# Kernel optimization log

Hardware: AMD Instinct MI355X
Metric: run time of the kernel (lower is better)

## Reference

```python
import jax, jax.numpy as jnp
import numpy as np

EPS = 1e-06


def setup_inputs() -> dict:
    key = jax.random.key(0)
    k1, k2, k3, k4 = jax.random.split(key, 4)
    b, n, h, w = 16, 32, 256, 256
    pd = jax.random.uniform(k1, (b, h, w), dtype=jnp.float32)
    gt = jax.random.uniform(k2, (b, h, w), dtype=jnp.float32)
    pd_mask = jax.random.randint(k3, (b, n, h, w), 0, 2, dtype=jnp.int32)
    gt_mask = jax.random.randint(k4, (b, n, h, w), 0, 2, dtype=jnp.int32)
    return {"pd": pd, "gt": gt, "pd_mask": pd_mask, "gt_mask": gt_mask}


def reference(pd, gt, pd_mask, gt_mask):
    pdm = pd_mask.astype(bool)
    gtm = gt_mask.astype(bool)
    and_m = jnp.logical_and(pdm, gtm)            # pd & gt
    xor_m = jnp.logical_and(pdm, jnp.logical_not(gtm))  # (pd|gt) ^ gt == pd & ~gt
    f = pd.dtype
    # segmented masked sums over (h,w) for every (b, n) instance, fully vectorized
    inter = jnp.einsum('bhw,bnhw->bn', pd, and_m.astype(f))
    union = (jnp.einsum('bhw,bnhw->bn', gt, gtm.astype(f))
             + jnp.einsum('bhw,bnhw->bn', pd, xor_m.astype(f)))
    loss = inter / (union + EPS)
    return 1.0 - jnp.mean(loss)
```

## Files before the change

kernel.cpp:

```cpp
#include <hip/hip_runtime.h>

#define B 16
#define N 32
#define HW 65536
#define CHUNKS 4
#define CHUNK (HW / CHUNKS)
#define PAIRS (B * N)
#define NBLK (PAIRS * CHUNKS)
#define EPS 1e-6f


__global__ __launch_bounds__(256, 4) void iou_partial_kernel(
    const float* __restrict__ pd, const float* __restrict__ gt,
    const int* __restrict__ pdm, const int* __restrict__ gtm,
    float2* __restrict__ ws)
{
    const int blk   = (blockIdx.x & 7) * (NBLK / 8) + (blockIdx.x >> 3);
    const int pair  = blk >> 2;
    const int chunk = blk & 3;
    const int b     = pair >> 5;
    const int t     = threadIdx.x;

    const int base = chunk * CHUNK;
    const float4* __restrict__ pdp = (const float4*)(pd + (size_t)b * HW + base);
    const float4* __restrict__ gtp = (const float4*)(gt + (size_t)b * HW + base);
    const int4*   __restrict__ pmp = (const int4*)(pdm + (size_t)pair * HW + base);
    const int4*   __restrict__ gmp = (const int4*)(gtm + (size_t)pair * HW + base);

    float inter = 0.0f, uni = 0.0f;

    #pragma unroll
    for (int o = 0; o < 4; ++o) {
        float4 p[4], g[4];
        int4  pm[4], gm[4];
        #pragma unroll
        for (int u = 0; u < 4; ++u) {
            const int i = (o * 4 + u) * 256 + t;
            pm[u] = pmp[i];
            gm[u] = gmp[i];
            p[u]  = pdp[i];
            g[u]  = gtp[i];
        }
        #pragma unroll
        for (int u = 0; u < 4; ++u) {
            inter += (pm[u].x & gm[u].x) ? p[u].x : 0.0f;
            inter += (pm[u].y & gm[u].y) ? p[u].y : 0.0f;
            inter += (pm[u].z & gm[u].z) ? p[u].z : 0.0f;
            inter += (pm[u].w & gm[u].w) ? p[u].w : 0.0f;

            uni += (gm[u].x ? g[u].x : 0.0f) + ((pm[u].x & ~gm[u].x) ? p[u].x : 0.0f);
            uni += (gm[u].y ? g[u].y : 0.0f) + ((pm[u].y & ~gm[u].y) ? p[u].y : 0.0f);
            uni += (gm[u].z ? g[u].z : 0.0f) + ((pm[u].z & ~gm[u].z) ? p[u].z : 0.0f);
            uni += (gm[u].w ? g[u].w : 0.0f) + ((pm[u].w & ~gm[u].w) ? p[u].w : 0.0f);
        }
    }

    #pragma unroll
    for (int o = 32; o > 0; o >>= 1) {
        inter += __shfl_down(inter, o, 64);
        uni   += __shfl_down(uni, o, 64);
    }

    __shared__ float s_i[4], s_u[4];
    const int wave = t >> 6, lane = t & 63;
    if (lane == 0) { s_i[wave] = inter; s_u[wave] = uni; }
    __syncthreads();
    if (t == 0) {
        ws[blk] = make_float2(s_i[0] + s_i[1] + s_i[2] + s_i[3],
                              s_u[0] + s_u[1] + s_u[2] + s_u[3]);
    }
}

__global__ __launch_bounds__(512) void iou_final_kernel(
    const float2* __restrict__ ws, float* __restrict__ out)
{
    const int t = threadIdx.x;
    float I = 0.0f, U = 0.0f;
    #pragma unroll
    for (int c = 0; c < CHUNKS; ++c) {
        float2 v = ws[t * CHUNKS + c];
        I += v.x; U += v.y;
    }
    float loss = I / (U + EPS);

    #pragma unroll
    for (int o = 32; o > 0; o >>= 1)
        loss += __shfl_down(loss, o, 64);

    __shared__ float s[8];
    const int wave = t >> 6, lane = t & 63;
    if (lane == 0) s[wave] = loss;
    __syncthreads();
    if (t == 0) {
        float sum = 0.0f;
        #pragma unroll
        for (int w = 0; w < 8; ++w) sum += s[w];
        out[0] = 1.0f - sum / (float)PAIRS;
    }
}

extern "C" void kernel_launch(void* const* d_in, const int* in_sizes, int n_in,
                              void* d_out, int out_size, void* d_ws, size_t ws_size,
                              hipStream_t stream) {
    const float* pd  = (const float*)d_in[0];
    const float* gt  = (const float*)d_in[1];
    const int*   pdm = (const int*)d_in[2];
    const int*   gtm = (const int*)d_in[3];
    float* out = (float*)d_out;
    float2* ws = (float2*)d_ws;

    iou_partial_kernel<<<NBLK, 256, 0, stream>>>(pd, gt, pdm, gtm, ws);
    iou_final_kernel<<<1, 512, 0, stream>>>(ws, out);
}
```

Before: 46.43 us.

## Reuse pd/gt chunks across all instances with register-pipelined mask loads

Each block now owns one spatial chunk of one batch item and loops over all 32 instances. It loads pd/gt once into registers and streams the mask tiles through a triple-buffered register prefetch. This removes the repeated reads of pd/gt for every instance, which were mostly L2 hits, and rebalances the grid to 512 blocks with more work per block. In exchange, register pressure rises (64 accumulators plus buffers, launch bounds occupancy 1), there are fewer blocks, and the final kernel has more partials to sum.

Result: slower. 82.77 us (+78.2%).

```diff
diff --git a/kernel.cpp b/kernel.cpp
--- a/kernel.cpp
+++ b/kernel.cpp
@@ -3,71 +3,92 @@
 #define B 16
 #define N 32
 #define HW 65536
-#define CHUNKS 4
-#define CHUNK (HW / CHUNKS)
+#define CHUNK 2048
+#define CPB (HW / CHUNK)
+#define NBLK (B * CPB)
 #define PAIRS (B * N)
-#define NBLK (PAIRS * CHUNKS)
+#define F4 (CHUNK / 4 / 256)
 #define EPS 1e-6f
 
 
-__global__ __launch_bounds__(256, 4) void iou_partial_kernel(
+__global__ __launch_bounds__(256, 1) void iou_partial_kernel(
     const float* __restrict__ pd, const float* __restrict__ gt,
     const int* __restrict__ pdm, const int* __restrict__ gtm,
     float2* __restrict__ ws)
 {
-    const int blk   = (blockIdx.x & 7) * (NBLK / 8) + (blockIdx.x >> 3);
-    const int pair  = blk >> 2;
-    const int chunk = blk & 3;
-    const int b     = pair >> 5;
+    const int blk   = blockIdx.x;
+    const int b     = blk >> 5;
+    const int chunk = blk & 31;
     const int t     = threadIdx.x;
+    const int base  = chunk * CHUNK;
 
-    const int base = chunk * CHUNK;
     const float4* __restrict__ pdp = (const float4*)(pd + (size_t)b * HW + base);
     const float4* __restrict__ gtp = (const float4*)(gt + (size_t)b * HW + base);
-    const int4*   __restrict__ pmp = (const int4*)(pdm + (size_t)pair * HW + base);
-    const int4*   __restrict__ gmp = (const int4*)(gtm + (size_t)pair * HW + base);
+    const int4*   __restrict__ pmp = (const int4*)(pdm + ((size_t)b * N) * HW + base);
+    const int4*   __restrict__ gmp = (const int4*)(gtm + ((size_t)b * N) * HW + base);
 
-    float inter = 0.0f, uni = 0.0f;
+    float4 p[F4], g[F4];
+    #pragma unroll
+    for (int u = 0; u < F4; ++u) {
+        p[u] = pdp[u * 256 + t];
+        g[u] = gtp[u * 256 + t];
+    }
+
+    float accI[N], accU[N];
+
+    int4 pmB[3][F4], gmB[3][F4];
+#define LOADM(slot, n)                                          \
+    {   const int _o = (n) * (HW / 4);                          \
+        _Pragma("unroll")                                       \
+        for (int u = 0; u < F4; ++u) {                          \
+            pmB[slot][u] = pmp[_o + u * 256 + t];               \
+            gmB[slot][u] = gmp[_o + u * 256 + t];               \
+        }                                                       \
+    }
+
+    LOADM(0, 0) LOADM(1, 1) LOADM(2, 2)
 
     #pragma unroll
-    for (int o = 0; o < 4; ++o) {
-        float4 p[4], g[4];
-        int4  pm[4], gm[4];
+    for (int n = 0; n < N; ++n) {
+        const int cur = n % 3;
+        float I = 0.0f, U = 0.0f;
         #pragma unroll
-        for (int u = 0; u < 4; ++u) {
-            const int i = (o * 4 + u) * 256 + t;
-            pm[u] = pmp[i];
-            gm[u] = gmp[i];
-            p[u]  = pdp[i];
-            g[u]  = gtp[i];
+        for (int u = 0; u < F4; ++u) {
+            const int4 pm = pmB[cur][u];
+            const int4 gm = gmB[cur][u];
+            I += (pm.x & gm.x) ? p[u].x : 0.0f;
+            I += (pm.y & gm.y) ? p[u].y : 0.0f;
+            I += (pm.z & gm.z) ? p[u].z : 0.0f;
+            I += (pm.w & gm.w) ? p[u].w : 0.0f;
+
+            U += (gm.x ? g[u].x : 0.0f) + ((pm.x & ~gm.x) ? p[u].x : 0.0f);
+            U += (gm.y ? g[u].y : 0.0f) + ((pm.y & ~gm.y) ? p[u].y : 0.0f);
+            U += (gm.z ? g[u].z : 0.0f) + ((pm.z & ~gm.z) ? p[u].z : 0.0f);
+            U += (gm.w ? g[u].w : 0.0f) + ((pm.w & ~gm.w) ? p[u].w : 0.0f);
         }
+        accI[n] = I;
+        accU[n] = U;
+        if (n + 3 < N) LOADM(cur, n + 3)
+    }
+#undef LOADM
+
+    __shared__ float sI[4][N], sU[4][N];
+    const int wave = t >> 6, lane = t & 63;
+    #pragma unroll
+    for (int n = 0; n < N; ++n) {
+        float I = accI[n], U = accU[n];
         #pragma unroll
-        for (int u = 0; u < 4; ++u) {
-            inter += (pm[u].x & gm[u].x) ? p[u].x : 0.0f;
-            inter += (pm[u].y & gm[u].y) ? p[u].y : 0.0f;
-            inter += (pm[u].z & gm[u].z) ? p[u].z : 0.0f;
-            inter += (pm[u].w & gm[u].w) ? p[u].w : 0.0f;
-
-            uni += (gm[u].x ? g[u].x : 0.0f) + ((pm[u].x & ~gm[u].x) ? p[u].x : 0.0f);
-            uni += (gm[u].y ? g[u].y : 0.0f) + ((pm[u].y & ~gm[u].y) ? p[u].y : 0.0f);
-            uni += (gm[u].z ? g[u].z : 0.0f) + ((pm[u].z & ~gm[u].z) ? p[u].z : 0.0f);
-            uni += (gm[u].w ? g[u].w : 0.0f) + ((pm[u].w & ~gm[u].w) ? p[u].w : 0.0f);
+        for (int o = 32; o > 0; o >>= 1) {
+            I += __shfl_down(I, o, 64);
+            U += __shfl_down(U, o, 64);
         }
+        if (lane == 0) { sI[wave][n] = I; sU[wave][n] = U; }
     }
-
-    #pragma unroll
-    for (int o = 32; o > 0; o >>= 1) {
-        inter += __shfl_down(inter, o, 64);
-        uni   += __shfl_down(uni, o, 64);
-    }
-
-    __shared__ float s_i[4], s_u[4];
-    const int wave = t >> 6, lane = t & 63;
-    if (lane == 0) { s_i[wave] = inter; s_u[wave] = uni; }
     __syncthreads();
-    if (t == 0) {
-        ws[blk] = make_float2(s_i[0] + s_i[1] + s_i[2] + s_i[3],
-                              s_u[0] + s_u[1] + s_u[2] + s_u[3]);
+    if (t < N) {
+        const float I = sI[0][t] + sI[1][t] + sI[2][t] + sI[3][t];
+        const float U = sU[0][t] + sU[1][t] + sU[2][t] + sU[3][t];
+        ws[((size_t)b * N + t) * CPB + chunk] = make_float2(I, U);
     }
 }
 
@@ -75,11 +96,13 @@
     const float2* __restrict__ ws, float* __restrict__ out)
 {
     const int t = threadIdx.x;
+    const float4* __restrict__ w4 = (const float4*)(ws + (size_t)t * CPB);
     float I = 0.0f, U = 0.0f;
     #pragma unroll
-    for (int c = 0; c < CHUNKS; ++c) {
-        float2 v = ws[t * CHUNKS + c];
-        I += v.x; U += v.y;
+    for (int c = 0; c < CPB / 2; ++c) {
+        const float4 v = w4[c];
+        I += v.x + v.z;
+        U += v.y + v.w;
     }
     float loss = I / (U + EPS);
 
```
